# Optimization experiments

Hardware: AMD Instinct MI355X
Metric: run time of the kernel (lower is better)

The kernel has to match this reference:

```python
import jax, jax.numpy as jnp
import numpy as np

B, N, TD, SD, BD, K, M, TOPK, H = 8, 1024, 5120, 2048, 1024, 16, 4, 2, 8
HD = SD // H  # 256


def _ln(x, g, b, eps=1e-5):
    m = jnp.mean(x, -1, keepdims=True)
    v = jnp.mean((x - m) ** 2, -1, keepdims=True)
    return (x - m) * jax.lax.rsqrt(v + eps) * g + b


def _adapter(h, dw, db, uw, ub, lg, lb, q, wq, bq, wk, bk, wv, bv, ow, ob, pg, pb):
    # bottleneck trunk: down -> GELU -> up -> LN (dropout = identity in eval)
    x = jax.nn.gelu(h @ dw + db, approximate=False)          # [B,N,BD]
    x = _ln(x @ uw + ub, lg, lb)                             # [B,N,SD]
    Bb = x.shape[0]
    # cross-attention: learnable queries [K,SD] attend over x
    qp = (q @ wq + bq).reshape(K, H, HD).transpose(1, 0, 2)                      # [H,K,HD]
    kp = (x @ wk + bk).reshape(Bb, -1, H, HD).transpose(0, 2, 1, 3)              # [B,H,N,HD]
    vp = (x @ wv + bv).reshape(Bb, -1, H, HD).transpose(0, 2, 1, 3)              # [B,H,N,HD]
    att = jax.nn.softmax(jnp.einsum('hkd,bhnd->bhkn', qp, kp) * (1.0 / np.sqrt(HD)), axis=-1)
    ctx = jnp.einsum('bhkn,bhnd->bhkd', att, vp).transpose(0, 2, 1, 3).reshape(Bb, K, SD)
    ctx = ctx @ ow + ob
    return _ln(ctx + q[None], pg, pb)                        # residual with queries


def setup_inputs():
    key = jax.random.key(0)
    it = iter(jax.random.split(key, 40))
    def nrm(shape, s=0.02):
        return jax.random.normal(next(it), shape, jnp.float32) * s
    inp = {'h_teacher': jax.random.normal(next(it), (B, N, TD), jnp.float32)}
    for pre, lead in (('g_', ()), ('s_', (M,))):
        inp[pre + 'dw'] = nrm(lead + (TD, BD)); inp[pre + 'db'] = jnp.zeros(lead + (BD,), jnp.float32)
        inp[pre + 'uw'] = nrm(lead + (BD, SD)); inp[pre + 'ub'] = jnp.zeros(lead + (SD,), jnp.float32)
        inp[pre + 'lg'] = jnp.ones(lead + (SD,), jnp.float32); inp[pre + 'lb'] = jnp.zeros(lead + (SD,), jnp.float32)
        inp[pre + 'q'] = nrm(lead + (K, SD))
        for nm in ('wq', 'wk', 'wv', 'ow'):
            inp[pre + nm] = nrm(lead + (SD, SD))
        for nm in ('bq', 'bk', 'bv', 'ob'):
            inp[pre + nm] = jnp.zeros(lead + (SD,), jnp.float32)
        inp[pre + 'pg'] = jnp.ones(lead + (SD,), jnp.float32); inp[pre + 'pb'] = jnp.zeros(lead + (SD,), jnp.float32)
    inp['r_w1'] = nrm((TD, 512)); inp['r_b1'] = jnp.zeros((512,), jnp.float32)
    inp['r_w2'] = nrm((512, M)); inp['r_b2'] = jnp.zeros((M,), jnp.float32)
    return inp


def reference(h_teacher, g_dw, g_db, g_uw, g_ub, g_lg, g_lb, g_q, g_wq, g_bq, g_wk, g_bk, g_wv, g_bv, g_ow, g_ob, g_pg, g_pb, s_dw, s_db, s_uw, s_ub, s_lg, s_lb, s_q, s_wq, s_bq, s_wk, s_bk, s_wv, s_bv, s_ow, s_ob, s_pg, s_pb, r_w1, r_b1, r_w2, r_b2):
    # generalized adapter (always on)
    c_g = _adapter(h_teacher, g_dw, g_db, g_uw, g_ub, g_lg, g_lb, g_q, g_wq, g_bq, g_wk, g_bk, g_wv, g_bv, g_ow, g_ob, g_pg, g_pb)
    # all specialized experts computed densely (as the torch module does), then gathered
    c_spec = jax.vmap(lambda dw, db, uw, ub, lg, lb, q, wq, bq, wk, bk, wv, bv, ow, ob, pg, pb:
                      _adapter(h_teacher, dw, db, uw, ub, lg, lb, q, wq, bq, wk, bk, wv, bv, ow, ob, pg, pb))(
        s_dw, s_db, s_uw, s_ub, s_lg, s_lb, s_q, s_wq, s_bq, s_wk, s_bk, s_wv, s_bv, s_ow, s_ob, s_pg, s_pb)  # [M,B,K,SD]
    cs = jnp.transpose(c_spec, (1, 0, 2, 3))                 # [B,M,K,SD]
    # router on mean-pooled teacher summary (eval: no noise)
    pooled = jnp.mean(h_teacher, axis=1)                     # [B,TD]
    logits = jax.nn.gelu(pooled @ r_w1 + r_b1, approximate=False) @ r_w2 + r_b2
    probs = jax.nn.softmax(logits, axis=-1)                  # [B,M]
    w, idx = jax.lax.top_k(probs, TOPK)                      # [B,TOPK]
    w = w / (jnp.sum(w, -1, keepdims=True) + 1e-8)
    sel = cs[jnp.arange(cs.shape[0])[:, None], idx]          # [B,TOPK,K,SD]
    c_s = jnp.sum(sel * w[:, :, None, None], axis=1)         # [B,K,SD]
    c_agg = jnp.concatenate([c_g, c_s], axis=1)              # [B,2K,SD]
    return c_agg, probs
```

## Files before the change

### kernel.cpp

```cpp
#include <hip/hip_runtime.h>
#include <hip/hip_bf16.h>

#define B_   8
#define N_   1024
#define TD_  5120
#define SD_  2048
#define BD_  1024
#define K_   16
#define H_   8

typedef unsigned short u16;
typedef __attribute__((ext_vector_type(8))) short bf16x8;
typedef __attribute__((ext_vector_type(4))) float f32x4;
typedef __attribute__((ext_vector_type(8))) u16 u16x8;

__device__ __forceinline__ float bf2f(u16 u) {
    union { unsigned int i; float f; } x; x.i = ((unsigned)u) << 16; return x.f;
}
__device__ __forceinline__ u16 f2bf(float f) {
    union { float f; unsigned int i; } x; x.f = f;
    unsigned int i = x.i;
    return (u16)((i + 0x7fffu + ((i >> 16) & 1u)) >> 16);
}
__device__ __forceinline__ float gelu_exact(float v) {
    return 0.5f * v * (1.0f + erff(v * 0.70710678118654752f));
}
__device__ __forceinline__ void gload_lds16(const void* g, void* l) {
    __builtin_amdgcn_global_load_lds(
        (const __attribute__((address_space(1))) unsigned int*)g,
        (__attribute__((address_space(3))) unsigned int*)l, 16, 0, 0);
}

struct Ptr5 { const float* p[5]; };
struct Ptr40 { const float* p[8][5]; };

template<int EPI, int AMODE>
__global__ __launch_bounds__(256, 2)
void gemm_units(const u16* __restrict__ Abase,
                const u16* __restrict__ Bbase, long bStride,
                const float* __restrict__ biasBase, int biasStride,
                u16* __restrict__ Cbase, int ldc, long cStride,
                int Kd, const int* __restrict__ units_a, const int* __restrict__ units_b)
{
    __shared__ u16 As[2*128*32];
    __shared__ u16 Bs[2*128*32];
    const int u = blockIdx.z;
    const int ua = units_a[u];
    const int ub = (AMODE == 0) ? units_b[u] : u;
    const u16* A  = Abase + (size_t)ub * 1024 * Kd;
    const u16* Bt = Bbase + (size_t)ua * bStride;
    const float* bias = biasBase + (size_t)ua * biasStride;
    u16* C = Cbase + (size_t)u * cStride;

    const int tid  = threadIdx.x;
    const int wave = tid >> 6, lane = tid & 63;
    const int row0 = blockIdx.x * 128, col0 = blockIdx.y * 128;
    const int wr = wave >> 1, wc = wave & 1;

    const int sr  = tid >> 2;
    const int cg  = (tid & 3) ^ ((sr >> 1) & 3);
    const char* aP0 = (const char*)(A  + (size_t)(row0 + sr)      * Kd + cg*8);
    const char* aP1 = (const char*)(A  + (size_t)(row0 + 64 + sr) * Kd + cg*8);
    const char* bP0 = (const char*)(Bt + (size_t)(col0 + sr)      * Kd + cg*8);
    const char* bP1 = (const char*)(Bt + (size_t)(col0 + 64 + sr) * Kd + cg*8);

    const int fr = lane & 15;
    const int chunk = (lane >> 4) ^ ((fr >> 1) & 3);
    int aoff[4], boff[4];
#pragma unroll
    for (int m = 0; m < 4; ++m) aoff[m] = (wr*64 + m*16 + fr)*32 + chunk*8;
#pragma unroll
    for (int n = 0; n < 4; ++n) boff[n] = (wc*64 + n*16 + fr)*32 + chunk*8;

    const int nkt = Kd >> 5;
    {
        char* asW = (char*)As + wave*1024;
        char* bsW = (char*)Bs + wave*1024;
        gload_lds16(aP0, asW);
        gload_lds16(aP1, asW + 4096);
        gload_lds16(bP0, bsW);
        gload_lds16(bP1, bsW + 4096);
    }
    asm volatile("s_waitcnt vmcnt(0)" ::: "memory");
    __syncthreads();

    f32x4 acc[4][4] = {};
    int cur = 0;
    for (int kt = 0; kt < nkt; ++kt) {
        if (kt + 1 < nkt) {
            const size_t kb = (size_t)(kt + 1) << 6;
            char* asN = (char*)As + (cur^1)*8192 + wave*1024;
            char* bsN = (char*)Bs + (cur^1)*8192 + wave*1024;
            gload_lds16(aP0 + kb, asN);
            gload_lds16(aP1 + kb, asN + 4096);
            gload_lds16(bP0 + kb, bsN);
            gload_lds16(bP1 + kb, bsN + 4096);
        }
        const u16* Ab = As + cur*4096;
        const u16* Bb = Bs + cur*4096;
        bf16x8 af[4], bfr[4];
#pragma unroll
        for (int m = 0; m < 4; ++m) af[m]  = *(const bf16x8*)(Ab + aoff[m]);
#pragma unroll
        for (int n = 0; n < 4; ++n) bfr[n] = *(const bf16x8*)(Bb + boff[n]);
#pragma unroll
        for (int m = 0; m < 4; ++m)
#pragma unroll
            for (int n = 0; n < 4; ++n)
                acc[m][n] = __builtin_amdgcn_mfma_f32_16x16x32_bf16(af[m], bfr[n], acc[m][n], 0, 0, 0);
        asm volatile("s_waitcnt vmcnt(0)" ::: "memory");
        __syncthreads();
        cur ^= 1;
    }

    const int fq = lane >> 4;
#pragma unroll
    for (int m = 0; m < 4; ++m)
#pragma unroll
        for (int n = 0; n < 4; ++n) {
            const int col = col0 + wc*64 + n*16 + fr;
            const float bv = bias[col];
#pragma unroll
            for (int j = 0; j < 4; ++j) {
                const int row = row0 + wr*64 + m*16 + fq*4 + j;
                float v = acc[m][n][j] + bv;
                if (EPI == 1) v = gelu_exact(v);
                C[(size_t)row*ldc + col] = f2bf(v);
            }
        }
}

__global__ void cvt_bf16_flat(const float* __restrict__ in, u16* __restrict__ out, long n8) {
    long i = (long)blockIdx.x * blockDim.x + threadIdx.x;
    const long stride = (long)gridDim.x * blockDim.x;
    for (; i < n8; i += stride) {
        const f32x4* p = (const f32x4*)in + i*2;
        f32x4 a = p[0], b = p[1];
        u16x8 o;
        o[0]=f2bf(a[0]); o[1]=f2bf(a[1]); o[2]=f2bf(a[2]); o[3]=f2bf(a[3]);
        o[4]=f2bf(b[0]); o[5]=f2bf(b[1]); o[6]=f2bf(b[2]); o[7]=f2bf(b[3]);
        ((u16x8*)out)[i] = o;
    }
}

__global__ __launch_bounds__(256)
void cvt_transpose(const float* __restrict__ W, u16* __restrict__ Wt, int Kd, int Nd) {
    __shared__ float t[64][65];
    const int k0 = blockIdx.x * 64, n0 = blockIdx.y * 64;
    const int tid = threadIdx.x;
#pragma unroll
    for (int i = 0; i < 4; ++i) {
        int ch = tid + i*256;
        int r = ch >> 4, c4 = (ch & 15) << 2;
        f32x4 v = *(const f32x4*)(W + (size_t)(k0 + r)*Nd + n0 + c4);
        t[r][c4] = v[0]; t[r][c4+1] = v[1]; t[r][c4+2] = v[2]; t[r][c4+3] = v[3];
    }
    __syncthreads();
#pragma unroll
    for (int i = 0; i < 2; ++i) {
        int ch = tid + i*256;
        int nr = ch >> 3, c8 = (ch & 7) << 3;
        u16x8 o;
#pragma unroll
        for (int j = 0; j < 8; ++j) o[j] = f2bf(t[c8 + j][nr]);
        *(u16x8*)(Wt + (size_t)(n0 + nr)*Kd + k0 + c8) = o;
    }
}

__global__ __launch_bounds__(256)
void ln_rows_u(u16* __restrict__ X, const float* __restrict__ gslab,
               const float* __restrict__ bslab, const int* __restrict__ units_a) {
    const int row = blockIdx.x, tid = threadIdx.x;
    const int ua = units_a[row >> 10];
    const float* g  = gslab + (size_t)ua*SD_;
    const float* bt = bslab + (size_t)ua*SD_;
    u16* rp = X + (size_t)row*SD_;
    const u16x8 v = ((const u16x8*)rp)[tid];
    float f[8]; float s = 0.f, s2 = 0.f;
#pragma unroll
    for (int j = 0; j < 8; ++j) { f[j] = bf2f(v[j]); s += f[j]; s2 += f[j]*f[j]; }
    __shared__ float sa[4], sb[4];
#pragma unroll
    for (int o = 32; o > 0; o >>= 1) { s += __shfl_down(s, o); s2 += __shfl_down(s2, o); }
    if ((tid & 63) == 0) { sa[tid >> 6] = s; sb[tid >> 6] = s2; }
    __syncthreads();
    s = sa[0]+sa[1]+sa[2]+sa[3]; s2 = sb[0]+sb[1]+sb[2]+sb[3];
    const float mean = s * (1.0f/SD_);
    const float inv  = rsqrtf(s2 * (1.0f/SD_) - mean*mean + 1e-5f);
    const int c0 = tid*8;
    u16x8 o;
#pragma unroll
    for (int j = 0; j < 8; ++j) o[j] = f2bf((f[j]-mean)*inv*g[c0+j] + bt[c0+j]);
    ((u16x8*)rp)[tid] = o;
}

__global__ __launch_bounds__(256)
void qp_part(Ptr5 q, Ptr5 wq, float* __restrict__ Sp) {
    __shared__ float qL[16][256];
    const int a = blockIdx.y, ks = blockIdx.z;
    const int c = blockIdx.x*256 + threadIdx.x;
    const int t = threadIdx.x;
    const float* Q = q.p[a];
    for (int i = t; i < 16*256; i += 256)
        qL[i >> 8][i & 255] = Q[(size_t)(i >> 8)*SD_ + ks*256 + (i & 255)];
    __syncthreads();
    const float* W = wq.p[a] + (size_t)(ks*256)*SD_ + c;
    float acc[16] = {};
    for (int i = 0; i < 256; i += 4) {
        const float w0 = W[(size_t)i*SD_];
        const float w1 = W[(size_t)(i+1)*SD_];
        const float w2 = W[(size_t)(i+2)*SD_];
        const float w3 = W[(size_t)(i+3)*SD_];
#pragma unroll
        for (int k = 0; k < 16; ++k) {
            f32x4 q4 = *(const f32x4*)&qL[k][i];
            acc[k] += q4[0]*w0 + q4[1]*w1 + q4[2]*w2 + q4[3]*w3;
        }
    }
#pragma unroll
    for (int k = 0; k < 16; ++k)
        Sp[((size_t)(a*8 + ks)*16 + k)*SD_ + c] = acc[k];
}

__global__ void qp_reduce(const float* __restrict__ Sp, Ptr5 bq, float* __restrict__ qp) {
    const int idx = blockIdx.x*256 + threadIdx.x;
    const int a = idx >> 15, k = (idx >> 11) & 15, c = idx & 2047;
    float s = bq.p[a][c];
#pragma unroll
    for (int ks = 0; ks < 8; ++ks)
        s += Sp[((size_t)(a*8 + ks)*16 + k)*SD_ + c];
    qp[idx] = s;
}

__global__ __launch_bounds__(256)
void scores_sm(const u16* __restrict__ Kb, const float* __restrict__ qp,
               const int* __restrict__ units_a, float* __restrict__ P)
{
    __shared__ float sL[16][1024];
    __shared__ float qL[16][256];
    __shared__ float red[8];
    const int u = blockIdx.x >> 3, hh = blockIdx.x & 7;
    const int ua = units_a[u];
    const int t = threadIdx.x;
    for (int i = t; i < 16*256; i += 256)
        qL[i >> 8][i & 255] = qp[(size_t)(ua*16 + (i >> 8))*SD_ + hh*256 + (i & 255)];
    __syncthreads();
    const u16* Ku = Kb + (size_t)u*1024*SD_ + hh*256;
#pragma unroll
    for (int j = 0; j < 4; ++j) {
        const int n = t + j*256;
        const u16* kr = Ku + (size_t)n*SD_;
        float acc[16] = {};
        for (int d0 = 0; d0 < 256; d0 += 8) {
            u16x8 kv8 = *(const u16x8*)(kr + d0);
            float kf[8];
#pragma unroll
            for (int e = 0; e < 8; ++e) kf[e] = bf2f(kv8[e]);
#pragma unroll
            for (int k = 0; k < 16; ++k) {
                f32x4 q0 = *(const f32x4*)&qL[k][d0];
                f32x4 q1 = *(const f32x4*)&qL[k][d0+4];
                acc[k] += q0[0]*kf[0] + q0[1]*kf[1] + q0[2]*kf[2] + q0[3]*kf[3]
                        + q1[0]*kf[4] + q1[1]*kf[5] + q1[2]*kf[6] + q1[3]*kf[7];
            }
        }
#pragma unroll
        for (int k = 0; k < 16; ++k) sL[k][n] = acc[k] * 0.0625f;
    }
    __syncthreads();
    const int lane = t & 63, wv = t >> 6;
    for (int k = 0; k < 16; ++k) {
        float v0 = sL[k][t], v1 = sL[k][t+256], v2 = sL[k][t+512], v3 = sL[k][t+768];
        float mx = fmaxf(fmaxf(v0,v1), fmaxf(v2,v3));
#pragma unroll
        for (int o = 1; o < 64; o <<= 1) mx = fmaxf(mx, __shfl_xor(mx, o));
        if (lane == 0) red[wv] = mx;
        __syncthreads();
        mx = fmaxf(fmaxf(red[0],red[1]), fmaxf(red[2],red[3]));
        float e0 = expf(v0-mx), e1 = expf(v1-mx), e2 = expf(v2-mx), e3 = expf(v3-mx);
        float s = e0+e1+e2+e3;
#pragma unroll
        for (int o = 1; o < 64; o <<= 1) s += __shfl_xor(s, o);
        if (lane == 0) red[4+wv] = s;
        __syncthreads();
        s = red[4]+red[5]+red[6]+red[7];
        const float inv = 1.0f/s;
        float* Pr = P + ((size_t)(u*8+hh)*16 + k)*1024;
        Pr[t]=e0*inv; Pr[t+256]=e1*inv; Pr[t+512]=e2*inv; Pr[t+768]=e3*inv;
        __syncthreads();
    }
}

__global__ __launch_bounds__(256)
void ctx_u(const u16* __restrict__ Vb, const float* __restrict__ P,
           u16* __restrict__ ctxb)
{
    __shared__ float pL[16][1024];
    const int u = blockIdx.x >> 3, hh = blockIdx.x & 7;
    const int t = threadIdx.x;
    const float* Pu = P + (size_t)(u*8+hh)*16*1024;
    for (int i = t; i < 16*1024/4; i += 256)
        ((f32x4*)&pL[0][0])[i] = ((const f32x4*)Pu)[i];
    __syncthreads();
    const u16* Vu = Vb + (size_t)u*1024*SD_ + hh*256 + t;
    float acc[16] = {};
    for (int n = 0; n < 1024; n += 4) {
        float vv0 = bf2f(Vu[(size_t)n*SD_]);
        float vv1 = bf2f(Vu[(size_t)(n+1)*SD_]);
        float vv2 = bf2f(Vu[(size_t)(n+2)*SD_]);
        float vv3 = bf2f(Vu[(size_t)(n+3)*SD_]);
#pragma unroll
        for (int k = 0; k < 16; ++k) {
            f32x4 p4 = *(const f32x4*)&pL[k][n];
            acc[k] += p4[0]*vv0 + p4[1]*vv1 + p4[2]*vv2 + p4[3]*vv3;
        }
    }
#pragma unroll
    for (int k = 0; k < 16; ++k)
        ctxb[(size_t)u*16*SD_ + k*SD_ + hh*256 + t] = f2bf(acc[k]);
}

__global__ __launch_bounds__(256)
void gemm_ow(const u16* __restrict__ ctxb, const u16* __restrict__ Bslab,
             const float* __restrict__ biasSlab, const int* __restrict__ units_a,
             float* __restrict__ ctx2)
{
    const int u = blockIdx.y, ua = units_a[u];
    const int wave = threadIdx.x >> 6, lane = threadIdx.x & 63;
    const int col0 = blockIdx.x*256 + wave*64;
    const u16* A  = ctxb + (size_t)u*16*SD_;
    const u16* Bt = Bslab + (size_t)ua*SD_*SD_;
    const int fr = lane & 15, fk8 = (lane >> 4) << 3;
    f32x4 acc[4] = {};
    for (int k0 = 0; k0 < SD_; k0 += 32) {
        bf16x8 af = *(const bf16x8*)(A + (size_t)fr*SD_ + k0 + fk8);
#pragma unroll
        for (int n = 0; n < 4; ++n) {
            bf16x8 bf8 = *(const bf16x8*)(Bt + (size_t)(col0 + n*16 + fr)*SD_ + k0 + fk8);
            acc[n] = __builtin_amdgcn_mfma_f32_16x16x32_bf16(af, bf8, acc[n], 0, 0, 0);
        }
    }
    const int fq = lane >> 4;
#pragma unroll
    for (int n = 0; n < 4; ++n)
#pragma unroll
        for (int j = 0; j < 4; ++j) {
            const int row = fq*4 + j, col = col0 + n*16 + fr;
            ctx2[(size_t)u*16*SD_ + (size_t)row*SD_ + col] = acc[n][j] + biasSlab[ua*SD_ + col];
        }
}

__global__ __launch_bounds__(256)
void ln_post_u(const float* __restrict__ ctx2, const float* __restrict__ qslab,
               const float* __restrict__ pgs, const float* __restrict__ pbs,
               const int* __restrict__ units_a, const int* __restrict__ units_b,
               float* __restrict__ out, float* __restrict__ cspec)
{
    const int k = blockIdx.x, u = blockIdx.y, tid = threadIdx.x;
    const int ua = units_a[u];
    const float* ip = ctx2 + ((size_t)u*16 + k)*SD_;
    const float* qr = qslab + ((size_t)ua*16 + k)*SD_;
    const float* g  = pgs + (size_t)ua*SD_;
    const float* bt = pbs + (size_t)ua*SD_;
    float f[8]; float s = 0.f, s2 = 0.f;
#pragma unroll
    for (int j = 0; j < 8; ++j) {
        const int c = tid + j*256;
        f[j] = ip[c] + qr[c];
        s += f[j]; s2 += f[j]*f[j];
    }
    __shared__ float sa[4], sb[4];
#pragma unroll
    for (int o = 32; o > 0; o >>= 1) { s += __shfl_down(s, o); s2 += __shfl_down(s2, o); }
    if ((tid & 63) == 0) { sa[tid >> 6] = s; sb[tid >> 6] = s2; }
    __syncthreads();
    s = sa[0]+sa[1]+sa[2]+sa[3]; s2 = sb[0]+sb[1]+sb[2]+sb[3];
    const float mean = s * (1.0f/SD_);
    const float inv  = rsqrtf(s2 * (1.0f/SD_) - mean*mean + 1e-5f);
    float* op = (u < 8) ? out + ((size_t)units_b[u]*32 + k)*SD_
                        : cspec + ((size_t)(u-8)*16 + k)*SD_;
#pragma unroll
    for (int j = 0; j < 8; ++j) { const int c = tid + j*256; op[c] = (f[j]-mean)*inv*g[c] + bt[c]; }
}

__global__ __launch_bounds__(256)
void pool_part(const float* __restrict__ h, float* __restrict__ pp) {
    const int c = blockIdx.x*256 + threadIdx.x;
    const int b = blockIdx.y, ns = blockIdx.z;
    const float* p = h + ((size_t)b*N_ + ns*256)*TD_ + c;
    float s = 0.f;
    for (int n = 0; n < 256; ++n) s += p[(size_t)n*TD_];
    pp[(size_t)ns*8*TD_ + (size_t)b*TD_ + c] = s;
}
__global__ void pool_reduce(const float* __restrict__ pp, float* __restrict__ pooled) {
    const int idx = blockIdx.x*256 + threadIdx.x;
    const float s = pp[idx] + pp[idx + 8*TD_] + pp[idx + 16*TD_] + pp[idx + 24*TD_];
    pooled[idx] = s * (1.0f/N_);
}

__global__ __launch_bounds__(256)
void rmlp_part(const float* __restrict__ pooled, const float* __restrict__ w1,
               float* __restrict__ rp) {
    const int c = blockIdx.x*256 + threadIdx.x;
    const int b = blockIdx.y, is = blockIdx.z;
    const float* pr = pooled + b*TD_ + is*512;
    const float* W = w1 + (size_t)(is*512)*512 + c;
    float s = 0.f;
    for (int i = 0; i < 512; ++i) s += pr[i] * W[(size_t)i*512];
    rp[(b*10 + is)*512 + c] = s;
}
__global__ void rmlp_reduce(const float* __restrict__ rp, const float* __restrict__ b1,
                            float* __restrict__ hid) {
    const int idx = blockIdx.x*256 + threadIdx.x;
    const int b = idx >> 9, c = idx & 511;
    float s = b1[c];
#pragma unroll
    for (int is = 0; is < 10; ++is) s += rp[(b*10 + is)*512 + c];
    hid[idx] = gelu_exact(s);
}

__global__ void router_final(const float* __restrict__ hid, const float* __restrict__ w2,
                             const float* __restrict__ b2, float* __restrict__ probs,
                             int* __restrict__ widx, float* __restrict__ wval,
                             int* __restrict__ units_a, int* __restrict__ units_b) {
    __shared__ float lg[8][4];
    __shared__ int sw[16];
    const int tid = threadIdx.x;
    if (tid < 32) {
        const int b = tid >> 2, m = tid & 3;
        float s = b2[m];
        const float* hr = hid + b*512;
        for (int i = 0; i < 512; ++i) s += hr[i]*w2[i*4 + m];
        lg[b][m] = s;
    }
    __syncthreads();
    if (tid < 8) {
        const int b = tid;
        const float l0=lg[b][0], l1=lg[b][1], l2=lg[b][2], l3=lg[b][3];
        const float mx = fmaxf(fmaxf(l0,l1),fmaxf(l2,l3));
        const float e0=expf(l0-mx), e1=expf(l1-mx), e2=expf(l2-mx), e3=expf(l3-mx);
        const float s = e0+e1+e2+e3;
        float p[4] = {e0/s, e1/s, e2/s, e3/s};
        probs[b*4+0]=p[0]; probs[b*4+1]=p[1]; probs[b*4+2]=p[2]; probs[b*4+3]=p[3];
        int i0 = 0;
        for (int m = 1; m < 4; ++m) if (p[m] > p[i0]) i0 = m;
        int i1 = -1;
        for (int m = 0; m < 4; ++m) if (m != i0 && (i1 < 0 || p[m] > p[i1])) i1 = m;
        const float w0 = p[i0], w1 = p[i1], ws = w0 + w1 + 1e-8f;
        widx[b*2]=i0; widx[b*2+1]=i1;
        wval[b*2]=w0/ws; wval[b*2+1]=w1/ws;
        sw[b*2]=i0; sw[b*2+1]=i1;
    }
    __syncthreads();
    if (tid < 24) {
        units_a[tid] = (tid < 8) ? 0 : sw[tid-8] + 1;
        units_b[tid] = (tid < 8) ? tid : ((tid-8) >> 1);
    }
}

__global__ void combine_k(const float* __restrict__ cspec, const int* __restrict__ widx,
                          const float* __restrict__ wval, float* __restrict__ out) {
    const int i = blockIdx.x*256 + threadIdx.x;
    const int c4 = i & 511;
    const int k  = (i >> 9) & 15;
    const int b  = i >> 13;
    const float w0 = wval[b*2], w1 = wval[b*2+1];
    const f32x4 v0 = ((const f32x4*)cspec)[(size_t)((2*b)  *16 + k)*512 + c4];
    const f32x4 v1 = ((const f32x4*)cspec)[(size_t)((2*b+1)*16 + k)*512 + c4];
    ((f32x4*)out)[(size_t)(b*32 + 16 + k)*512 + c4] = v0*w0 + v1*w1;
}

__global__ void pack5(Ptr5 src, float* __restrict__ dst, int len) {
    int i = blockIdx.x*256 + threadIdx.x;
    if (i < 5*len) dst[i] = src.p[i/len][i%len];
}
__global__ void pack_slab8(Ptr40 s, float* __restrict__ dst) {
    int i = blockIdx.x*256 + threadIdx.x;
    int slab = i / 10240, rem = i % 10240;
    dst[i] = s.p[slab][rem / 2048][rem % 2048];
}

extern "C" void kernel_launch(void* const* d_in, const int* in_sizes, int n_in,
                              void* d_out, int out_size, void* d_ws, size_t ws_size,
                              hipStream_t stream) {
    if (ws_size < 300300000ULL) return;

    const float* h = (const float*)d_in[0];
    const float* G[17]; const float* Sx[17];
    for (int i = 0; i < 17; ++i) { G[i] = (const float*)d_in[1+i]; Sx[i] = (const float*)d_in[18+i]; }
    const float* r_w1 = (const float*)d_in[35];
    const float* r_b1 = (const float*)d_in[36];
    const float* r_w2 = (const float*)d_in[37];
    const float* r_b2 = (const float*)d_in[38];

    static const size_t str[17] = {
        (size_t)TD_*BD_, BD_, (size_t)BD_*SD_, SD_, SD_, SD_, (size_t)K_*SD_,
        (size_t)SD_*SD_, (size_t)SD_*SD_, (size_t)SD_*SD_, (size_t)SD_*SD_,
        SD_, SD_, SD_, SD_, SD_, SD_ };
    auto P = [&](int pi, int a) -> const float* {
        return (a == 0) ? G[pi] : Sx[pi] + (size_t)(a-1)*str[pi];
    };

    char* w = (char*)d_ws;
    const size_t R0 = 0, R1 = 100663296, R2 = 201326592, R3 = 251658240, TAIL = 293601280;
    u16*   h_bf  = (u16*)(w + R0);
    u16*   X     = (u16*)(w + R0);
    u16*   wt_dw = (u16*)(w + R1);
    u16*   Kbuf  = (u16*)(w + R1);
    u16*   X1    = (u16*)(w + R2);
    u16*   wt_v  = (u16*)(w + R2);
    u16*   wt_ow = (u16*)(w + R2);
    u16*   wt_uw = (u16*)(w + R3);
    u16*   wt_k  = (u16*)(w + R3);
    u16*   ctxb  = (u16*)(w + R3);
    float* ctx2  = (float*)(w + R3 + 1572864);
    float* cspec = (float*)(w + R3 + 4718592);
    float* Pbuf  = (float*)(w + R3 + 6815744);
    float* qpp   = (float*)(w + R2);
    float* poolp = (float*)(w + R2 + 12582912);
    float* routp = (float*)(w + R2 + 14680064);
    float* qp_all  = (float*)(w + TAIL);
    float* qslab   = (float*)(w + TAIL + 655360);
    float* bias_dw = (float*)(w + TAIL + 1310720);
    float* slab8   = (float*)(w + TAIL + 1331200);
    float* pooled  = (float*)(w + TAIL + 1658880);
    float* hid     = (float*)(w + TAIL + 1822720);
    int*   widx    = (int*)  (w + TAIL + 1839104);
    float* wval    = (float*)(w + TAIL + 1839168);
    int*   units_a = (int*)  (w + TAIL + 1839232);
    int*   units_b = (int*)  (w + TAIL + 1839328);

    float* bias_uw = slab8;
    float* bias_k  = slab8 + 1*5*SD_;
    float* bias_v  = slab8 + 2*5*SD_;
    float* bias_ow = slab8 + 3*5*SD_;
    float* lng     = slab8 + 4*5*SD_;
    float* lnb     = slab8 + 5*5*SD_;
    float* pgs     = slab8 + 6*5*SD_;
    float* pbs     = slab8 + 7*5*SD_;

    float* out = (float*)d_out;

    cvt_bf16_flat<<<2048, 256, 0, stream>>>(h, h_bf, (long)((size_t)B_*N_*TD_/8));
    pool_part<<<dim3(20, 8, 4), 256, 0, stream>>>(h, poolp);
    pool_reduce<<<160, 256, 0, stream>>>(poolp, pooled);
    rmlp_part<<<dim3(2, 8, 10), 256, 0, stream>>>(pooled, r_w1, routp);
    rmlp_reduce<<<16, 256, 0, stream>>>(routp, r_b1, hid);
    router_final<<<1, 64, 0, stream>>>(hid, r_w2, r_b2, out + 524288, widx, wval, units_a, units_b);

    Ptr5 q5, wq5, bq5, db5;
    for (int a = 0; a < 5; ++a) { q5.p[a]=P(6,a); wq5.p[a]=P(7,a); bq5.p[a]=P(11,a); db5.p[a]=P(1,a); }
    qp_part<<<dim3(8, 5, 8), 256, 0, stream>>>(q5, wq5, qpp);
    qp_reduce<<<640, 256, 0, stream>>>(qpp, bq5, qp_all);
    pack5<<<20, 256, 0, stream>>>(db5, bias_dw, BD_);
    pack5<<<640, 256, 0, stream>>>(q5, qslab, 16*SD_);
    Ptr40 s8;
    static const int slab_pi[8] = {3, 12, 13, 14, 4, 5, 15, 16};
    for (int si = 0; si < 8; ++si)
        for (int a = 0; a < 5; ++a) s8.p[si][a] = P(slab_pi[si], a);
    pack_slab8<<<320, 256, 0, stream>>>(s8, slab8);

    for (int a = 0; a < 5; ++a) {
        cvt_transpose<<<dim3(TD_/64, BD_/64), 256, 0, stream>>>(P(0,a), wt_dw + (size_t)a*BD_*TD_, TD_, BD_);
        cvt_transpose<<<dim3(BD_/64, SD_/64), 256, 0, stream>>>(P(2,a), wt_uw + (size_t)a*SD_*BD_, BD_, SD_);
    }

    gemm_units<1, 0><<<dim3(8, 8, 24), 256, 0, stream>>>(
        h_bf, wt_dw, (long)BD_*TD_, bias_dw, BD_, X1, BD_, (long)1024*BD_, TD_, units_a, units_b);

    gemm_units<0, 1><<<dim3(8, 16, 24), 256, 0, stream>>>(
        X1, wt_uw, (long)SD_*BD_, bias_uw, SD_, X, SD_, (long)1024*SD_, BD_, units_a, units_b);

    ln_rows_u<<<24*1024, 256, 0, stream>>>(X, lng, lnb, units_a);

    for (int a = 0; a < 5; ++a) {
        cvt_transpose<<<dim3(SD_/64, SD_/64), 256, 0, stream>>>(P(8,a), wt_k + (size_t)a*SD_*SD_, SD_, SD_);
        cvt_transpose<<<dim3(SD_/64, SD_/64), 256, 0, stream>>>(P(9,a), wt_v + (size_t)a*SD_*SD_, SD_, SD_);
    }

    gemm_units<0, 1><<<dim3(8, 16, 24), 256, 0, stream>>>(
        X, wt_k, (long)SD_*SD_, bias_k, SD_, Kbuf, SD_, (long)1024*SD_, SD_, units_a, units_b);

    scores_sm<<<24*8, 256, 0, stream>>>(Kbuf, qp_all, units_a, Pbuf);

    gemm_units<0, 1><<<dim3(8, 16, 24), 256, 0, stream>>>(
        X, wt_v, (long)SD_*SD_, bias_v, SD_, Kbuf, SD_, (long)1024*SD_, SD_, units_a, units_b);

    for (int a = 0; a < 5; ++a)
        cvt_transpose<<<dim3(SD_/64, SD_/64), 256, 0, stream>>>(P(10,a), wt_ow + (size_t)a*SD_*SD_, SD_, SD_);

    ctx_u<<<24*8, 256, 0, stream>>>(Kbuf, Pbuf, ctxb);

    gemm_ow<<<dim3(8, 24), 256, 0, stream>>>(ctxb, wt_ow, bias_ow, units_a, ctx2);

    ln_post_u<<<dim3(16, 24), 256, 0, stream>>>(ctx2, qslab, pgs, pbs, units_a, units_b, out, cspec);
    combine_k<<<256, 256, 0, stream>>>(cspec, widx, wval, out);
}
```

Baseline: 1.604 ms.

## Replace 128x128 GEMM with 256x256 tile, 8-wave kernel and interleaved LDS pipeline

The batched bf16 GEMM used for the down, up, K and V projections now uses 256x256 output tiles with 512 threads, a K-step of 64, and 128 KB of double-buffered LDS with XOR swizzling. The main loop interleaves asynchronous global-to-LDS staging of the next tile with LDS fragment reads and MFMA bursts, using s_setprio and fine-grained barriers. The aim is more operand reuse per byte loaded and better overlap of memory traffic with matrix math. In exchange, the large LDS footprint limits residency to one block per CU. The grid also shrinks to 384 or 768 blocks, which may leave partial waves of work at the tail.

Result: faster. 1.441 ms (-10.2%).

```diff
diff --git a/kernel.cpp b/kernel.cpp
--- a/kernel.cpp
+++ b/kernel.cpp
@@ -35,15 +35,14 @@
 struct Ptr40 { const float* p[8][5]; };
 
 template<int EPI, int AMODE>
-__global__ __launch_bounds__(256, 2)
-void gemm_units(const u16* __restrict__ Abase,
-                const u16* __restrict__ Bbase, long bStride,
-                const float* __restrict__ biasBase, int biasStride,
-                u16* __restrict__ Cbase, int ldc, long cStride,
-                int Kd, const int* __restrict__ units_a, const int* __restrict__ units_b)
+__global__ __launch_bounds__(512, 2)
+void gemm256(const u16* __restrict__ Abase,
+             const u16* __restrict__ Bbase, long bStride,
+             const float* __restrict__ biasBase, int biasStride,
+             u16* __restrict__ Cbase, int ldc, long cStride, int Kd,
+             const int* __restrict__ units_a, const int* __restrict__ units_b)
 {
-    __shared__ u16 As[2*128*32];
-    __shared__ u16 Bs[2*128*32];
+    __shared__ char lds[131072];
     const int u = blockIdx.z;
     const int ua = units_a[u];
     const int ub = (AMODE == 0) ? units_b[u] : u;
@@ -54,76 +53,113 @@
 
     const int tid  = threadIdx.x;
     const int wave = tid >> 6, lane = tid & 63;
-    const int row0 = blockIdx.x * 128, col0 = blockIdx.y * 128;
-    const int wr = wave >> 1, wc = wave & 1;
-
-    const int sr  = tid >> 2;
-    const int cg  = (tid & 3) ^ ((sr >> 1) & 3);
-    const char* aP0 = (const char*)(A  + (size_t)(row0 + sr)      * Kd + cg*8);
-    const char* aP1 = (const char*)(A  + (size_t)(row0 + 64 + sr) * Kd + cg*8);
-    const char* bP0 = (const char*)(Bt + (size_t)(col0 + sr)      * Kd + cg*8);
-    const char* bP1 = (const char*)(Bt + (size_t)(col0 + 64 + sr) * Kd + cg*8);
-
-    const int fr = lane & 15;
-    const int chunk = (lane >> 4) ^ ((fr >> 1) & 3);
-    int aoff[4], boff[4];
-#pragma unroll
-    for (int m = 0; m < 4; ++m) aoff[m] = (wr*64 + m*16 + fr)*32 + chunk*8;
-#pragma unroll
-    for (int n = 0; n < 4; ++n) boff[n] = (wc*64 + n*16 + fr)*32 + chunk*8;
-
-    const int nkt = Kd >> 5;
+    const int wm = wave >> 2, wn = wave & 3;
+    const int row0 = blockIdx.x * 256, col0 = blockIdx.y * 256;
+
+    const int srow = tid >> 3;
+    const int scol = ((tid & 7) ^ ((tid >> 3) & 7)) << 3;
+    const char* aSrc = (const char*)(A  + (size_t)(row0 + srow) * Kd + scol);
+    const char* bSrc = (const char*)(Bt + (size_t)(col0 + srow) * Kd + scol);
+    const int ldsW = wave * 1024;
+
+    const int fr = lane & 15, fq = lane >> 4;
+    const int kl  = fq << 4;
+    const int swz = (fr & 7) << 4;
+
+    f32x4 acc[8][4] = {};
+    bf16x8 aF[4], bF[4];
+
+#define STAGE_A(bufv, hh, kt) do { \
+    const char* s_ = aSrc + ((size_t)((hh)*128) * Kd + (size_t)(kt) * 64) * 2; \
+    char* d_ = lds + (bufv)*65536 + (hh)*16384 + ldsW; \
+    gload_lds16(s_, d_); \
+    gload_lds16(s_ + (size_t)64 * Kd * 2, d_ + 8192); } while(0)
+#define STAGE_B(bufv, hh, kt) do { \
+    const char* s_ = bSrc + ((size_t)((hh)*128) * Kd + (size_t)(kt) * 64) * 2; \
+    char* d_ = lds + (bufv)*65536 + 32768 + (hh)*16384 + ldsW; \
+    gload_lds16(s_, d_); \
+    gload_lds16(s_ + (size_t)64 * Kd * 2, d_ + 8192); } while(0)
+
+#define LDA_(bufv, mf, kk) (*(const bf16x8*)(lds + (bufv)*65536 + \
+    ((mf)*32 + wm*16 + fr)*128 + ((((kk)*64) + kl) ^ swz)))
+#define LDB_(bufv, nf, kk) (*(const bf16x8*)(lds + (bufv)*65536 + 32768 + \
+    (wn*64 + (nf)*16 + fr)*128 + ((((kk)*64) + kl) ^ swz)))
+
+#define FENCE_ asm volatile("" ::: "memory")
+#define BAR_   __builtin_amdgcn_s_barrier()
+#define WAITL_ asm volatile("s_waitcnt lgkmcnt(0)" ::: "memory")
+#define VM_(n) asm volatile("s_waitcnt vmcnt(" #n ")" ::: "memory")
+
+#define READ_B(bufv, kk) { _Pragma("unroll") \
+    for (int n_ = 0; n_ < 4; ++n_) bF[n_] = LDB_(bufv, n_, kk); }
+#define READ_A(bufv, mh, kk) { _Pragma("unroll") \
+    for (int i_ = 0; i_ < 4; ++i_) aF[i_] = LDA_(bufv, (mh)*4 + i_, kk); }
+#define MFMA_(mh) { __builtin_amdgcn_s_setprio(1); \
+    _Pragma("unroll") for (int i_ = 0; i_ < 4; ++i_) { \
+      _Pragma("unroll") for (int n_ = 0; n_ < 4; ++n_) \
+        acc[(mh)*4+i_][n_] = __builtin_amdgcn_mfma_f32_16x16x32_bf16( \
+            aF[i_], bF[n_], acc[(mh)*4+i_][n_], 0, 0, 0); } \
+    __builtin_amdgcn_s_setprio(0); }
+
+    STAGE_A(0, 0, 0);
+    STAGE_B(0, 0, 0);
+    STAGE_B(0, 1, 0);
+    STAGE_A(0, 1, 0);
+
+    const int nt = Kd >> 6;
+    for (int T = 0; T < nt - 1; ++T) {
+        const int bufv = T & 1, nb = bufv ^ 1;
+        STAGE_A(nb, 0, T + 1);
+        VM_(4); BAR_; FENCE_;
+        READ_B(bufv, 0); READ_A(bufv, 0, 0);
+        WAITL_; MFMA_(0); BAR_;
+        STAGE_B(nb, 0, T + 1);
+        VM_(4); BAR_; FENCE_;
+        READ_A(bufv, 1, 0);
+        WAITL_; MFMA_(1); BAR_;
+        READ_B(bufv, 1); READ_A(bufv, 0, 1);
+        STAGE_B(nb, 1, T + 1);
+        BAR_; WAITL_; MFMA_(0); BAR_;
+        READ_A(bufv, 1, 1);
+        STAGE_A(nb, 1, T + 1);
+        BAR_; WAITL_; MFMA_(1); BAR_;
+    }
     {
-        char* asW = (char*)As + wave*1024;
-        char* bsW = (char*)Bs + wave*1024;
-        gload_lds16(aP0, asW);
-        gload_lds16(aP1, asW + 4096);
-        gload_lds16(bP0, bsW);
-        gload_lds16(bP1, bsW + 4096);
-    }
-    asm volatile("s_waitcnt vmcnt(0)" ::: "memory");
-    __syncthreads();
-
-    f32x4 acc[4][4] = {};
-    int cur = 0;
-    for (int kt = 0; kt < nkt; ++kt) {
-        if (kt + 1 < nkt) {
-            const size_t kb = (size_t)(kt + 1) << 6;
-            char* asN = (char*)As + (cur^1)*8192 + wave*1024;
-            char* bsN = (char*)Bs + (cur^1)*8192 + wave*1024;
-            gload_lds16(aP0 + kb, asN);
-            gload_lds16(aP1 + kb, asN + 4096);
-            gload_lds16(bP0 + kb, bsN);
-            gload_lds16(bP1 + kb, bsN + 4096);
-        }
-        const u16* Ab = As + cur*4096;
-        const u16* Bb = Bs + cur*4096;
-        bf16x8 af[4], bfr[4];
-#pragma unroll
-        for (int m = 0; m < 4; ++m) af[m]  = *(const bf16x8*)(Ab + aoff[m]);
-#pragma unroll
-        for (int n = 0; n < 4; ++n) bfr[n] = *(const bf16x8*)(Bb + boff[n]);
-#pragma unroll
-        for (int m = 0; m < 4; ++m)
-#pragma unroll
-            for (int n = 0; n < 4; ++n)
-                acc[m][n] = __builtin_amdgcn_mfma_f32_16x16x32_bf16(af[m], bfr[n], acc[m][n], 0, 0, 0);
-        asm volatile("s_waitcnt vmcnt(0)" ::: "memory");
-        __syncthreads();
-        cur ^= 1;
-    }
-
-    const int fq = lane >> 4;
-#pragma unroll
-    for (int m = 0; m < 4; ++m)
-#pragma unroll
-        for (int n = 0; n < 4; ++n) {
-            const int col = col0 + wc*64 + n*16 + fr;
+        const int bufv = (nt - 1) & 1;
+        VM_(2); BAR_; FENCE_;
+        READ_B(bufv, 0); READ_A(bufv, 0, 0);
+        WAITL_; MFMA_(0); BAR_;
+        VM_(0); BAR_; FENCE_;
+        READ_A(bufv, 1, 0);
+        WAITL_; MFMA_(1);
+        READ_B(bufv, 1); READ_A(bufv, 0, 1);
+        WAITL_; MFMA_(0);
+        READ_A(bufv, 1, 1);
+        WAITL_; MFMA_(1);
+    }
+
+#undef STAGE_A
+#undef STAGE_B
+#undef LDA_
+#undef LDB_
+#undef FENCE_
+#undef BAR_
+#undef WAITL_
+#undef VM_
+#undef READ_B
+#undef READ_A
+#undef MFMA_
+
+#pragma unroll
+    for (int mf = 0; mf < 8; ++mf)
+#pragma unroll
+        for (int nf = 0; nf < 4; ++nf) {
+            const int col = col0 + wn*64 + nf*16 + fr;
             const float bv = bias[col];
 #pragma unroll
             for (int j = 0; j < 4; ++j) {
-                const int row = row0 + wr*64 + m*16 + fq*4 + j;
-                float v = acc[m][n][j] + bv;
+                const int row = row0 + mf*32 + wm*16 + fq*4 + j;
+                float v = acc[mf][nf][j] + bv;
                 if (EPI == 1) v = gelu_exact(v);
                 C[(size_t)row*ldc + col] = f2bf(v);
             }
@@ -565,10 +601,10 @@
         cvt_transpose<<<dim3(BD_/64, SD_/64), 256, 0, stream>>>(P(2,a), wt_uw + (size_t)a*SD_*BD_, BD_, SD_);
     }
 
-    gemm_units<1, 0><<<dim3(8, 8, 24), 256, 0, stream>>>(
+    gemm256<1, 0><<<dim3(4, 4, 24), 512, 0, stream>>>(
         h_bf, wt_dw, (long)BD_*TD_, bias_dw, BD_, X1, BD_, (long)1024*BD_, TD_, units_a, units_b);
 
-    gemm_units<0, 1><<<dim3(8, 16, 24), 256, 0, stream>>>(
+    gemm256<0, 1><<<dim3(4, 8, 24), 512, 0, stream>>>(
         X1, wt_uw, (long)SD_*BD_, bias_uw, SD_, X, SD_, (long)1024*SD_, BD_, units_a, units_b);
 
     ln_rows_u<<<24*1024, 256, 0, stream>>>(X, lng, lnb, units_a);
@@ -578,12 +614,12 @@
         cvt_transpose<<<dim3(SD_/64, SD_/64), 256, 0, stream>>>(P(9,a), wt_v + (size_t)a*SD_*SD_, SD_, SD_);
     }
 
-    gemm_units<0, 1><<<dim3(8, 16, 24), 256, 0, stream>>>(
+    gemm256<0, 1><<<dim3(4, 8, 24), 512, 0, stream>>>(
         X, wt_k, (long)SD_*SD_, bias_k, SD_, Kbuf, SD_, (long)1024*SD_, SD_, units_a, units_b);
 
     scores_sm<<<24*8, 256, 0, stream>>>(Kbuf, qp_all, units_a, Pbuf);
 
-    gemm_units<0, 1><<<dim3(8, 16, 24), 256, 0, stream>>>(
+    gemm256<0, 1><<<dim3(4, 8, 24), 512, 0, stream>>>(
         X, wt_v, (long)SD_*SD_, bias_v, SD_, Kbuf, SD_, (long)1024*SD_, SD_, units_a, units_b);
 
     for (int a = 0; a < 5; ++a)
```

## Restructure GEMM to single-buffered K=64 tiles with XOR swizzle and higher occupancy

Applied to the files above, without the earlier changes.

Replaces the double-buffered K=32 GEMM main loop with a single-buffered loop that loads K=64 tiles (32 KB of LDS) per iteration and computes two MFMA k-steps per barrier. It uses a new XOR swizzle over 128-byte rows and raises launch_bounds from 2 to 4 blocks per CU. The aim is to halve the number of barriers and waits per unit of K and to rely on occupancy rather than software prefetch to hide latency. The cost is that loads no longer overlap compute within a block, and the higher occupancy target may squeeze registers for the 64 fp32 accumulators.

Result: faster. 1.475 ms (-8.1%).

```diff
diff --git a/kernel.cpp b/kernel.cpp
--- a/kernel.cpp
+++ b/kernel.cpp
@@ -35,15 +35,14 @@
 struct Ptr40 { const float* p[8][5]; };
 
 template<int EPI, int AMODE>
-__global__ __launch_bounds__(256, 2)
-void gemm_units(const u16* __restrict__ Abase,
-                const u16* __restrict__ Bbase, long bStride,
-                const float* __restrict__ biasBase, int biasStride,
-                u16* __restrict__ Cbase, int ldc, long cStride,
-                int Kd, const int* __restrict__ units_a, const int* __restrict__ units_b)
+__global__ __launch_bounds__(256, 4)
+void gemm128(const u16* __restrict__ Abase,
+             const u16* __restrict__ Bbase, long bStride,
+             const float* __restrict__ biasBase, int biasStride,
+             u16* __restrict__ Cbase, int ldc, long cStride, int Kd,
+             const int* __restrict__ units_a, const int* __restrict__ units_b)
 {
-    __shared__ u16 As[2*128*32];
-    __shared__ u16 Bs[2*128*32];
+    __shared__ char lds[32768];
     const int u = blockIdx.z;
     const int ua = units_a[u];
     const int ub = (AMODE == 0) ? units_b[u] : u;
@@ -54,76 +53,67 @@
 
     const int tid  = threadIdx.x;
     const int wave = tid >> 6, lane = tid & 63;
+    const int wm = wave >> 1, wn = wave & 1;
     const int row0 = blockIdx.x * 128, col0 = blockIdx.y * 128;
-    const int wr = wave >> 1, wc = wave & 1;
-
-    const int sr  = tid >> 2;
-    const int cg  = (tid & 3) ^ ((sr >> 1) & 3);
-    const char* aP0 = (const char*)(A  + (size_t)(row0 + sr)      * Kd + cg*8);
-    const char* aP1 = (const char*)(A  + (size_t)(row0 + 64 + sr) * Kd + cg*8);
-    const char* bP0 = (const char*)(Bt + (size_t)(col0 + sr)      * Kd + cg*8);
-    const char* bP1 = (const char*)(Bt + (size_t)(col0 + 64 + sr) * Kd + cg*8);
-
-    const int fr = lane & 15;
-    const int chunk = (lane >> 4) ^ ((fr >> 1) & 3);
-    int aoff[4], boff[4];
-#pragma unroll
-    for (int m = 0; m < 4; ++m) aoff[m] = (wr*64 + m*16 + fr)*32 + chunk*8;
-#pragma unroll
-    for (int n = 0; n < 4; ++n) boff[n] = (wc*64 + n*16 + fr)*32 + chunk*8;
-
-    const int nkt = Kd >> 5;
-    {
-        char* asW = (char*)As + wave*1024;
-        char* bsW = (char*)Bs + wave*1024;
-        gload_lds16(aP0, asW);
-        gload_lds16(aP1, asW + 4096);
-        gload_lds16(bP0, bsW);
-        gload_lds16(bP1, bsW + 4096);
-    }
-    asm volatile("s_waitcnt vmcnt(0)" ::: "memory");
-    __syncthreads();
+
+    const int srow = tid >> 3;
+    const int scol = ((tid & 7) ^ (srow & 7)) << 3;
+    const char* aSrc = (const char*)(A  + (size_t)(row0 + srow) * Kd + scol);
+    const char* bSrc = (const char*)(Bt + (size_t)(col0 + srow) * Kd + scol);
+    const int ldsW = wave * 1024;
+
+    const int fr = lane & 15, fq = lane >> 4;
+    const int kl  = fq << 4;
+    const int swz = (fr & 7) << 4;
 
     f32x4 acc[4][4] = {};
-    int cur = 0;
-    for (int kt = 0; kt < nkt; ++kt) {
-        if (kt + 1 < nkt) {
-            const size_t kb = (size_t)(kt + 1) << 6;
-            char* asN = (char*)As + (cur^1)*8192 + wave*1024;
-            char* bsN = (char*)Bs + (cur^1)*8192 + wave*1024;
-            gload_lds16(aP0 + kb, asN);
-            gload_lds16(aP1 + kb, asN + 4096);
-            gload_lds16(bP0 + kb, bsN);
-            gload_lds16(bP1 + kb, bsN + 4096);
-        }
-        const u16* Ab = As + cur*4096;
-        const u16* Bb = Bs + cur*4096;
-        bf16x8 af[4], bfr[4];
-#pragma unroll
-        for (int m = 0; m < 4; ++m) af[m]  = *(const bf16x8*)(Ab + aoff[m]);
-#pragma unroll
-        for (int n = 0; n < 4; ++n) bfr[n] = *(const bf16x8*)(Bb + boff[n]);
-#pragma unroll
-        for (int m = 0; m < 4; ++m)
-#pragma unroll
-            for (int n = 0; n < 4; ++n)
-                acc[m][n] = __builtin_amdgcn_mfma_f32_16x16x32_bf16(af[m], bfr[n], acc[m][n], 0, 0, 0);
+
+#define LDA_(mf, kk) (*(const bf16x8*)(lds + \
+    (wm*64 + (mf)*16 + fr)*128 + ((((kk)*64) + kl) ^ swz)))
+#define LDB_(nf, kk) (*(const bf16x8*)(lds + 16384 + \
+    (wn*64 + (nf)*16 + fr)*128 + ((((kk)*64) + kl) ^ swz)))
+
+    const int nt = Kd >> 6;
+    for (int T = 0; T < nt; ++T) {
+        const size_t kb = (size_t)T << 7;
+#pragma unroll
+        for (int l = 0; l < 4; ++l)
+            gload_lds16(aSrc + (size_t)(l*32)*Kd*2 + kb, lds + l*4096 + ldsW);
+#pragma unroll
+        for (int l = 0; l < 4; ++l)
+            gload_lds16(bSrc + (size_t)(l*32)*Kd*2 + kb, lds + 16384 + l*4096 + ldsW);
         asm volatile("s_waitcnt vmcnt(0)" ::: "memory");
         __syncthreads();
-        cur ^= 1;
-    }
-
-    const int fq = lane >> 4;
-#pragma unroll
-    for (int m = 0; m < 4; ++m)
-#pragma unroll
-        for (int n = 0; n < 4; ++n) {
-            const int col = col0 + wc*64 + n*16 + fr;
+#pragma unroll
+        for (int kk = 0; kk < 2; ++kk) {
+            bf16x8 aF[4], bF[4];
+#pragma unroll
+            for (int i = 0; i < 4; ++i) aF[i] = LDA_(i, kk);
+#pragma unroll
+            for (int n = 0; n < 4; ++n) bF[n] = LDB_(n, kk);
+#pragma unroll
+            for (int i = 0; i < 4; ++i)
+#pragma unroll
+                for (int n = 0; n < 4; ++n)
+                    acc[i][n] = __builtin_amdgcn_mfma_f32_16x16x32_bf16(
+                        aF[i], bF[n], acc[i][n], 0, 0, 0);
+        }
+        __syncthreads();
+    }
+
+#undef LDA_
+#undef LDB_
+
+#pragma unroll
+    for (int mf = 0; mf < 4; ++mf)
+#pragma unroll
+        for (int nf = 0; nf < 4; ++nf) {
+            const int col = col0 + wn*64 + nf*16 + fr;
             const float bv = bias[col];
 #pragma unroll
             for (int j = 0; j < 4; ++j) {
-                const int row = row0 + wr*64 + m*16 + fq*4 + j;
-                float v = acc[m][n][j] + bv;
+                const int row = row0 + wm*64 + mf*16 + fq*4 + j;
+                float v = acc[mf][nf][j] + bv;
                 if (EPI == 1) v = gelu_exact(v);
                 C[(size_t)row*ldc + col] = f2bf(v);
             }
@@ -565,10 +555,10 @@
         cvt_transpose<<<dim3(BD_/64, SD_/64), 256, 0, stream>>>(P(2,a), wt_uw + (size_t)a*SD_*BD_, BD_, SD_);
     }
 
-    gemm_units<1, 0><<<dim3(8, 8, 24), 256, 0, stream>>>(
+    gemm128<1, 0><<<dim3(8, 8, 24), 256, 0, stream>>>(
         h_bf, wt_dw, (long)BD_*TD_, bias_dw, BD_, X1, BD_, (long)1024*BD_, TD_, units_a, units_b);
 
-    gemm_units<0, 1><<<dim3(8, 16, 24), 256, 0, stream>>>(
+    gemm128<0, 1><<<dim3(8, 16, 24), 256, 0, stream>>>(
         X1, wt_uw, (long)SD_*BD_, bias_uw, SD_, X, SD_, (long)1024*SD_, BD_, units_a, units_b);
 
     ln_rows_u<<<24*1024, 256, 0, stream>>>(X, lng, lnb, units_a);
@@ -578,12 +568,12 @@
         cvt_transpose<<<dim3(SD_/64, SD_/64), 256, 0, stream>>>(P(9,a), wt_v + (size_t)a*SD_*SD_, SD_, SD_);
     }
 
-    gemm_units<0, 1><<<dim3(8, 16, 24), 256, 0, stream>>>(
+    gemm128<0, 1><<<dim3(8, 16, 24), 256, 0, stream>>>(
         X, wt_k, (long)SD_*SD_, bias_k, SD_, Kbuf, SD_, (long)1024*SD_, SD_, units_a, units_b);
 
     scores_sm<<<24*8, 256, 0, stream>>>(Kbuf, qp_all, units_a, Pbuf);
 
-    gemm_units<0, 1><<<dim3(8, 16, 24), 256, 0, stream>>>(
+    gemm128<0, 1><<<dim3(8, 16, 24), 256, 0, stream>>>(
         X, wt_v, (long)SD_*SD_, bias_v, SD_, Kbuf, SD_, (long)1024*SD_, SD_, units_a, units_b);
 
     for (int a = 0; a < 5; ++a)
```
